# Performance work log

Hardware: AMD Instinct MI355X
Metric: run time of the kernel (lower is better)

The kernel has to match this reference:

```python
import jax, jax.numpy as jnp
import numpy as np

PAD = -2.0 ** 16 + 1.0  # tf code uses -2**16+1 as masked logit
ITERATIONS = 3


def squash(x):
    # x: [..., out_units]
    n = jnp.sum(jnp.square(x), axis=-1, keepdims=True)
    return (n / (1.0 + n) / jnp.sqrt(n + 1e-9)) * x


def setup_inputs() -> dict:
    key = jax.random.key(0)
    k1, k2, k3, k4 = jax.random.split(key, 4)
    B, L, DIN, DOUT, K = 4096, 200, 64, 64, 8
    return {
        "low_capsule": jax.random.normal(k1, (B, L, DIN), dtype=jnp.float32),
        "seq_len": jax.random.randint(k2, (B, 1), 1, L + 1, dtype=jnp.int32),
        "B_matrix": jax.random.normal(k3, (1, K, L), dtype=jnp.float32),
        "S_matrix": jax.random.normal(k4, (DIN, DOUT), dtype=jnp.float32),
    }


def reference(low_capsule, seq_len, B_matrix, S_matrix):
    # low_capsule: [B, L, Din]; seq_len: [B, 1]; B_matrix: [1, K, L]; S_matrix: [Din, Dout]
    L = B_matrix.shape[2]
    # tf.sequence_mask(tile(seq_len,[1,K]), L) -> [B, K, L]; K axis broadcasts.
    mask = jnp.arange(L)[None, None, :] < seq_len[:, :, None]  # [B, 1, L]
    # low_capsule_new is identical every iteration; compute once.
    low_new = jnp.einsum('bli,io->blo', low_capsule, S_matrix)  # [B, L, Dout]
    Bc = B_matrix  # routing logits, updated (stateful assign_add in tf)
    high = None
    for _ in range(ITERATIONS):
        logits = jnp.where(mask, Bc, PAD)  # [B, K, L]
        W = jax.nn.softmax(logits, axis=-1)
        high = squash(jnp.einsum('bkl,blo->bko', W, low_new))  # [B, K, Dout]
        # B_delta = sum_b high @ low_new^T, keepdims on batch
        Bc = Bc + jnp.einsum('bko,blo->kl', high, low_new)[None]  # [1, K, L]
    return high
```

## Files before the change

### kernel.cpp

```cpp
#include <hip/hip_runtime.h>
#include <math.h>


#define B_SZ  4096
#define L_SZ  200
#define DINK  64
#define DOUTK 64
#define K_SZ  8

__global__ __launch_bounds__(256) void k_init(const float* __restrict__ Bm,
                                              float* __restrict__ Bc) {
    int i = blockIdx.x * 256 + threadIdx.x;
    if (i < K_SZ * L_SZ) Bc[i] = Bm[i];
}

template<int WRITE_OUT>
__global__ __launch_bounds__(256) void k_route(const float* __restrict__ lc_g,
                                               const int* __restrict__ seq_len,
                                               const float* __restrict__ S_g,
                                               const float* __restrict__ Bc,
                                               float* __restrict__ partial,
                                               float* __restrict__ out) {
    __shared__ float W_s[K_SZ][L_SZ];
    __shared__ float Ss[64][65];
    __shared__ float hp_s[K_SZ][DINK];
    __shared__ float hx_s[K_SZ][DOUTK];
    __shared__ float hs_s[K_SZ][DINK];
    int t = threadIdx.x;
    int b = blockIdx.x;
    long lbase = (long)b * (L_SZ * DINK);
    const float2* lc2 = (const float2*)(lc_g + lbase);
    int sl = seq_len[b];
    int k = t >> 5, g = t & 31;

    {
        const float4* S4 = (const float4*)S_g;
        for (int j = t; j < 1024; j += 256) {
            float4 v = S4[j];
            int r = j >> 4, c = (j & 15) * 4;
            Ss[r][c] = v.x; Ss[r][c+1] = v.y; Ss[r][c+2] = v.z; Ss[r][c+3] = v.w;
        }
    }

    const float* bk = Bc + k * L_SZ;
    float m = -3.4e38f;
    for (int l = g; l < sl; l += 32) m = fmaxf(m, bk[l]);
    #pragma unroll
    for (int s = 16; s > 0; s >>= 1) m = fmaxf(m, __shfl_xor(m, s, 32));
    float sum = 0.f;
    for (int l = g; l < sl; l += 32) {
        float e = __expf(bk[l] - m);
        sum += e;
        W_s[k][l] = e;
    }
    #pragma unroll
    for (int s = 16; s > 0; s >>= 1) sum += __shfl_xor(sum, s, 32);
    float rinv = 1.0f / sum;
    __syncthreads();

    {
        float a0 = 0.f, a1 = 0.f;
        for (int l = 0; l < sl; ++l) {
            float w = W_s[k][l];
            float2 v = lc2[l * 32 + g];
            a0 += w * v.x; a1 += w * v.y;
        }
        *(float2*)&hp_s[k][2 * g] = make_float2(a0 * rinv, a1 * rinv);
    }
    __syncthreads();

    {
        float h0 = 0.f, h1 = 0.f;
        #pragma unroll 8
        for (int i = 0; i < DINK; ++i) {
            float p = hp_s[k][i];
            float2 sv = *(const float2*)&Ss[i][2 * g];
            h0 += p * sv.x; h1 += p * sv.y;
        }
        float nn = h0 * h0 + h1 * h1;
        #pragma unroll
        for (int s = 16; s > 0; s >>= 1) nn += __shfl_xor(nn, s, 32);
        float sc = nn / ((1.0f + nn) * sqrtf(nn + 1e-9f));
        h0 *= sc; h1 *= sc;
        if (WRITE_OUT) {
            float2* ob2 = (float2*)(out + (long)b * (K_SZ * DOUTK) + k * DOUTK);
            ob2[g] = make_float2(h0, h1);
            return;
        }
        *(float2*)&hx_s[k][2 * g] = make_float2(h0, h1);
    }
    __syncthreads();

    {
        float s0 = 0.f, s1 = 0.f;
        int i0 = 2 * g, i1 = 2 * g + 1;
        #pragma unroll 8
        for (int o = 0; o < DOUTK; ++o) {
            float hv = hx_s[k][o];
            s0 += hv * Ss[i0][o];
            s1 += hv * Ss[i1][o];
        }
        *(float2*)&hs_s[k][2 * g] = make_float2(s0, s1);
    }
    __syncthreads();

    if (t < L_SZ) {
        const float4* row4 = (const float4*)(lc_g + lbase + (long)t * DINK);
        float* pb = partial + (long)b * (K_SZ * L_SZ);
        float acc[K_SZ] = {};
        #pragma unroll
        for (int i4 = 0; i4 < 16; ++i4) {
            float4 v = row4[i4];
            #pragma unroll
            for (int kk = 0; kk < K_SZ; ++kk) {
                float4 h = *(const float4*)&hs_s[kk][i4 * 4];
                acc[kk] += v.x * h.x + v.y * h.y + v.z * h.z + v.w * h.w;
            }
        }
        #pragma unroll
        for (int kk = 0; kk < K_SZ; ++kk)
            pb[kk * L_SZ + t] = acc[kk];
    }
}

__global__ __launch_bounds__(256) void k_reduceA(const float* __restrict__ partial,
                                                 float* __restrict__ partial2) {
    __shared__ float red[256];
    int x = blockIdx.x % 50;
    int y = blockIdx.x / 50;
    int t = threadIdx.x;
    int i = x * 32 + (t & 31);
    int sub = t >> 5;
    float s = 0.f;
    for (int p = y * 256 + sub; p < (y + 1) * 256; p += 8)
        s += partial[(long)p * (K_SZ * L_SZ) + i];
    red[t] = s;
    __syncthreads();
    for (int step = 4; step >= 1; step >>= 1) {
        if (sub < step) red[t] += red[t + step * 32];
        __syncthreads();
    }
    if (sub == 0) partial2[y * (K_SZ * L_SZ) + i] = red[t];
}

__global__ __launch_bounds__(256) void k_reduceB(const float* __restrict__ partial2,
                                                 float* __restrict__ Bc) {
    int i = blockIdx.x * 256 + threadIdx.x;
    if (i < K_SZ * L_SZ) {
        float s = 0.f;
        #pragma unroll
        for (int y = 0; y < 16; ++y) s += partial2[y * (K_SZ * L_SZ) + i];
        Bc[i] += s;
    }
}

extern "C" void kernel_launch(void* const* d_in, const int* in_sizes, int n_in,
                              void* d_out, int out_size, void* d_ws, size_t ws_size,
                              hipStream_t stream) {
    const float* lc = (const float*)d_in[0];
    const int*   sl = (const int*)d_in[1];
    const float* Bm = (const float*)d_in[2];
    const float* S  = (const float*)d_in[3];
    float* out = (float*)d_out;
    float* ws  = (float*)d_ws;

    float* Bc      = ws;
    float* partial = ws + 1600;
    float* p2      = out;

    k_init<<<7, 256, 0, stream>>>(Bm, Bc);

    k_route<0><<<B_SZ, 256, 0, stream>>>(lc, sl, S, Bc, partial, out);
    k_reduceA <<<800, 256, 0, stream>>>(partial, p2);
    k_reduceB <<<7, 256, 0, stream>>>(p2, Bc);
    k_route<0><<<B_SZ, 256, 0, stream>>>(lc, sl, S, Bc, partial, out);
    k_reduceA <<<800, 256, 0, stream>>>(partial, p2);
    k_reduceB <<<7, 256, 0, stream>>>(p2, Bc);
    k_route<1><<<B_SZ, 256, 0, stream>>>(lc, sl, S, Bc, partial, out);
}
```

Baseline: 304.4 us.

## Split weighted sum over L chunks so each low_capsule row is read once

The weighted-sum stage changes from each warp (one per capsule k) streaming all L rows of low_capsule to each warp handling interleaved 4-row chunks of L and accumulating all 8 capsules at once. Each row is then loaded from global memory once per block instead of eight times. Per-chunk partials go into a shared buffer that aliases the S matrix tile and are reduced across warps afterwards, so the S load is moved after that reduction. The cost is two extra barriers and more registers for the 8 float2 accumulators.

```diff
diff --git a/kernel.cpp b/kernel.cpp
--- a/kernel.cpp
+++ b/kernel.cpp
@@ -22,25 +22,19 @@
                                                float* __restrict__ partial,
                                                float* __restrict__ out) {
     __shared__ float W_s[K_SZ][L_SZ];
-    __shared__ float Ss[64][65];
+    __shared__ float ovl[64 * 65];
     __shared__ float hp_s[K_SZ][DINK];
     __shared__ float hx_s[K_SZ][DOUTK];
     __shared__ float hs_s[K_SZ][DINK];
+    float (*hp_part)[K_SZ][DINK] = (float (*)[K_SZ][DINK])ovl;
+    float (*Ss)[65] = (float (*)[65])ovl;
+
     int t = threadIdx.x;
     int b = blockIdx.x;
     long lbase = (long)b * (L_SZ * DINK);
     const float2* lc2 = (const float2*)(lc_g + lbase);
     int sl = seq_len[b];
     int k = t >> 5, g = t & 31;
-
-    {
-        const float4* S4 = (const float4*)S_g;
-        for (int j = t; j < 1024; j += 256) {
-            float4 v = S4[j];
-            int r = j >> 4, c = (j & 15) * 4;
-            Ss[r][c] = v.x; Ss[r][c+1] = v.y; Ss[r][c+2] = v.z; Ss[r][c+3] = v.w;
-        }
-    }
 
     const float* bk = Bc + k * L_SZ;
     float m = -3.4e38f;
@@ -59,13 +53,60 @@
     __syncthreads();
 
     {
-        float a0 = 0.f, a1 = 0.f;
-        for (int l = 0; l < sl; ++l) {
-            float w = W_s[k][l];
-            float2 v = lc2[l * 32 + g];
-            a0 += w * v.x; a1 += w * v.y;
-        }
-        *(float2*)&hp_s[k][2 * g] = make_float2(a0 * rinv, a1 * rinv);
+        float2 acc[K_SZ];
+        #pragma unroll
+        for (int kk = 0; kk < K_SZ; ++kk) acc[kk] = make_float2(0.f, 0.f);
+        int c = k;
+        for (int j = 0;; ++j) {
+            int l = 32 * j + 4 * c;
+            if (l >= sl) break;
+            if (l + 4 <= sl) {
+                float2 v0 = lc2[(l + 0) * 32 + g];
+                float2 v1 = lc2[(l + 1) * 32 + g];
+                float2 v2 = lc2[(l + 2) * 32 + g];
+                float2 v3 = lc2[(l + 3) * 32 + g];
+                #pragma unroll
+                for (int kk = 0; kk < K_SZ; ++kk) {
+                    float4 w = *(const float4*)&W_s[kk][l];
+                    acc[kk].x += w.x * v0.x + w.y * v1.x + w.z * v2.x + w.w * v3.x;
+                    acc[kk].y += w.x * v0.y + w.y * v1.y + w.z * v2.y + w.w * v3.y;
+                }
+            } else {
+                for (int u = l; u < sl; ++u) {
+                    float2 v = lc2[u * 32 + g];
+                    #pragma unroll
+                    for (int kk = 0; kk < K_SZ; ++kk) {
+                        float w = W_s[kk][u];
+                        acc[kk].x += w * v.x; acc[kk].y += w * v.y;
+                    }
+                }
+            }
+        }
+        #pragma unroll
+        for (int kk = 0; kk < K_SZ; ++kk)
+            *(float2*)&hp_part[c][kk][2 * g] = acc[kk];
+    }
+    __syncthreads();
+
+    {
+        float2 r = make_float2(0.f, 0.f);
+        #pragma unroll
+        for (int c = 0; c < K_SZ; ++c) {
+            float2 p = *(const float2*)&hp_part[c][k][2 * g];
+            r.x += p.x; r.y += p.y;
+        }
+        r.x *= rinv; r.y *= rinv;
+        *(float2*)&hp_s[k][2 * g] = r;
+    }
+    __syncthreads();
+
+    {
+        const float4* S4 = (const float4*)S_g;
+        for (int j = t; j < 1024; j += 256) {
+            float4 v = S4[j];
+            int r = j >> 4, cc = (j & 15) * 4;
+            Ss[r][cc] = v.x; Ss[r][cc+1] = v.y; Ss[r][cc+2] = v.z; Ss[r][cc+3] = v.w;
+        }
     }
     __syncthreads();
 
```

Result: slower. 356.9 us (+17.2%).

## Share low-capsule loads across all K routes and drop shared S staging

Applied to the files above, without the earlier changes.

The weighted sum over L is restructured so each thread owns one input column and accumulates all 8 routes at once, with 4 row-groups summed through shared memory. Previously each route's warp streamed the whole low_capsule tile on its own, so every block read it 8 times. The S matrix is no longer copied into shared memory per block. Instead the kernel reads S and a transposed copy, made once in k_init, from global/L2. Shared buffers are overlaid to cut the LDS footprint, and one barrier is removed, which adds an extra reduction step and global reads of S in exchange.

```diff
diff --git a/kernel.cpp b/kernel.cpp
--- a/kernel.cpp
+++ b/kernel.cpp
@@ -9,44 +9,46 @@
 #define K_SZ  8
 
 __global__ __launch_bounds__(256) void k_init(const float* __restrict__ Bm,
-                                              float* __restrict__ Bc) {
+                                              const float* __restrict__ S,
+                                              float* __restrict__ Bc,
+                                              float* __restrict__ St) {
     int i = blockIdx.x * 256 + threadIdx.x;
     if (i < K_SZ * L_SZ) Bc[i] = Bm[i];
+    int j = i - K_SZ * L_SZ;
+    if (j >= 0 && j < DINK * DOUTK) {
+        int o = j >> 6, ii = j & 63;
+        St[j] = S[ii * DOUTK + o];
+    }
 }
 
 template<int WRITE_OUT>
 __global__ __launch_bounds__(256) void k_route(const float* __restrict__ lc_g,
                                                const int* __restrict__ seq_len,
                                                const float* __restrict__ S_g,
+                                               const float* __restrict__ St_g,
                                                const float* __restrict__ Bc,
                                                float* __restrict__ partial,
                                                float* __restrict__ out) {
     __shared__ float W_s[K_SZ][L_SZ];
-    __shared__ float Ss[64][65];
     __shared__ float hp_s[K_SZ][DINK];
-    __shared__ float hx_s[K_SZ][DOUTK];
-    __shared__ float hs_s[K_SZ][DINK];
+    __shared__ float ovl[4 * K_SZ * DINK];
+    float (*hp_part)[K_SZ][DINK] = (float (*)[K_SZ][DINK])ovl;
+    float (*hx_s)[DINK] = (float (*)[DINK])(ovl);
+    float (*hs_s)[DINK] = (float (*)[DINK])(ovl + K_SZ * DINK);
+
     int t = threadIdx.x;
     int b = blockIdx.x;
     long lbase = (long)b * (L_SZ * DINK);
-    const float2* lc2 = (const float2*)(lc_g + lbase);
+    const float* lcb = lc_g + lbase;
     int sl = seq_len[b];
     int k = t >> 5, g = t & 31;
-
-    {
-        const float4* S4 = (const float4*)S_g;
-        for (int j = t; j < 1024; j += 256) {
-            float4 v = S4[j];
-            int r = j >> 4, c = (j & 15) * 4;
-            Ss[r][c] = v.x; Ss[r][c+1] = v.y; Ss[r][c+2] = v.z; Ss[r][c+3] = v.w;
-        }
-    }
+    int w = t >> 6, c = t & 63;
 
     const float* bk = Bc + k * L_SZ;
     float m = -3.4e38f;
     for (int l = g; l < sl; l += 32) m = fmaxf(m, bk[l]);
     #pragma unroll
-    for (int s = 16; s > 0; s >>= 1) m = fmaxf(m, __shfl_xor(m, s, 32));
+    for (int s = 16; s; s >>= 1) m = fmaxf(m, __shfl_xor(m, s, 32));
     float sum = 0.f;
     for (int l = g; l < sl; l += 32) {
         float e = __expf(bk[l] - m);
@@ -54,32 +56,61 @@
         W_s[k][l] = e;
     }
     #pragma unroll
-    for (int s = 16; s > 0; s >>= 1) sum += __shfl_xor(sum, s, 32);
+    for (int s = 16; s; s >>= 1) sum += __shfl_xor(sum, s, 32);
     float rinv = 1.0f / sum;
     __syncthreads();
 
     {
-        float a0 = 0.f, a1 = 0.f;
-        for (int l = 0; l < sl; ++l) {
-            float w = W_s[k][l];
-            float2 v = lc2[l * 32 + g];
-            a0 += w * v.x; a1 += w * v.y;
-        }
-        *(float2*)&hp_s[k][2 * g] = make_float2(a0 * rinv, a1 * rinv);
+        float acc[K_SZ];
+        #pragma unroll
+        for (int kk = 0; kk < K_SZ; ++kk) acc[kk] = 0.f;
+        for (int l = 4 * w; l < sl; l += 16) {
+            if (l + 4 <= sl) {
+                float v0 = lcb[(l + 0) * DINK + c];
+                float v1 = lcb[(l + 1) * DINK + c];
+                float v2 = lcb[(l + 2) * DINK + c];
+                float v3 = lcb[(l + 3) * DINK + c];
+                #pragma unroll
+                for (int kk = 0; kk < K_SZ; ++kk) {
+                    float4 w4 = *(const float4*)&W_s[kk][l];
+                    acc[kk] += w4.x * v0 + w4.y * v1 + w4.z * v2 + w4.w * v3;
+                }
+            } else {
+                for (int u = l; u < sl; ++u) {
+                    float v = lcb[u * DINK + c];
+                    #pragma unroll
+                    for (int kk = 0; kk < K_SZ; ++kk) acc[kk] += W_s[kk][u] * v;
+                }
+            }
+        }
+        #pragma unroll
+        for (int kk = 0; kk < K_SZ; ++kk) hp_part[w][kk][c] = acc[kk];
+    }
+    __syncthreads();
+
+    {
+        float2 r = make_float2(0.f, 0.f);
+        #pragma unroll
+        for (int cc = 0; cc < 4; ++cc) {
+            float2 p = *(const float2*)&hp_part[cc][k][2 * g];
+            r.x += p.x; r.y += p.y;
+        }
+        *(float2*)&hp_s[k][2 * g] = make_float2(r.x * rinv, r.y * rinv);
     }
     __syncthreads();
 
     {
         float h0 = 0.f, h1 = 0.f;
+        const float* sp = S_g + 2 * g;
         #pragma unroll 8
         for (int i = 0; i < DINK; ++i) {
             float p = hp_s[k][i];
-            float2 sv = *(const float2*)&Ss[i][2 * g];
+            float2 sv = *(const float2*)(sp + i * DOUTK);
             h0 += p * sv.x; h1 += p * sv.y;
         }
         float nn = h0 * h0 + h1 * h1;
         #pragma unroll
-        for (int s = 16; s > 0; s >>= 1) nn += __shfl_xor(nn, s, 32);
+        for (int s = 16; s; s >>= 1) nn += __shfl_xor(nn, s, 32);
         float sc = nn / ((1.0f + nn) * sqrtf(nn + 1e-9f));
         h0 *= sc; h1 *= sc;
         if (WRITE_OUT) {
@@ -89,23 +120,22 @@
         }
         *(float2*)&hx_s[k][2 * g] = make_float2(h0, h1);
     }
-    __syncthreads();
 
     {
         float s0 = 0.f, s1 = 0.f;
-        int i0 = 2 * g, i1 = 2 * g + 1;
+        const float* stp = St_g + 2 * g;
         #pragma unroll 8
         for (int o = 0; o < DOUTK; ++o) {
             float hv = hx_s[k][o];
-            s0 += hv * Ss[i0][o];
-            s1 += hv * Ss[i1][o];
+            float2 sv = *(const float2*)(stp + o * DINK);
+            s0 += hv * sv.x; s1 += hv * sv.y;
         }
         *(float2*)&hs_s[k][2 * g] = make_float2(s0, s1);
     }
     __syncthreads();
 
     if (t < L_SZ) {
-        const float4* row4 = (const float4*)(lc_g + lbase + (long)t * DINK);
+        const float4* row4 = (const float4*)(lcb + (long)t * DINK);
         float* pb = partial + (long)b * (K_SZ * L_SZ);
         float acc[K_SZ] = {};
         #pragma unroll
@@ -165,16 +195,17 @@
     float* ws  = (float*)d_ws;
 
     float* Bc      = ws;
-    float* partial = ws + 1600;
+    float* St      = ws + 1600;
+    float* partial = St + 4096;
     float* p2      = out;
 
-    k_init<<<7, 256, 0, stream>>>(Bm, Bc);
-
-    k_route<0><<<B_SZ, 256, 0, stream>>>(lc, sl, S, Bc, partial, out);
+    k_init<<<23, 256, 0, stream>>>(Bm, S, Bc, St);
+
+    k_route<0><<<B_SZ, 256, 0, stream>>>(lc, sl, S, St, Bc, partial, out);
     k_reduceA <<<800, 256, 0, stream>>>(partial, p2);
     k_reduceB <<<7, 256, 0, stream>>>(p2, Bc);
-    k_route<0><<<B_SZ, 256, 0, stream>>>(lc, sl, S, Bc, partial, out);
+    k_route<0><<<B_SZ, 256, 0, stream>>>(lc, sl, S, St, Bc, partial, out);
     k_reduceA <<<800, 256, 0, stream>>>(partial, p2);
     k_reduceB <<<7, 256, 0, stream>>>(p2, Bc);
-    k_route<1><<<B_SZ, 256, 0, stream>>>(lc, sl, S, Bc, partial, out);
-}
+    k_route<1><<<B_SZ, 256, 0, stream>>>(lc, sl, S, St, Bc, partial, out);
+}
```

Measured after the change: 287.4 us. -5.6%, faster.
